# Performance work log

Hardware: AMD Instinct MI355X
Metric: run time of the kernel (lower is better)

Reference implementation:

```python
import jax, jax.numpy as jnp
import numpy as np

N_NODES = 100000
N_EDGES = 600000
D = 128
N_LAYERS = 3
N_GRAPHS = 64
LN_EPS = 1e-5


def setup_inputs() -> dict:
    key = jax.random.key(0)
    ks = jax.random.split(key, 10)
    x = jax.random.normal(ks[0], (N_NODES, D), dtype=jnp.float32)
    edge_index = jax.random.randint(ks[1], (2, N_EDGES), 0, N_NODES, dtype=jnp.int32)
    batch_ids = jnp.sort(jax.random.randint(ks[2], (N_NODES,), 0, N_GRAPHS, dtype=jnp.int32))
    s = 1.0 / np.sqrt(D)
    proj_W = jax.random.normal(ks[3], (D, D), dtype=jnp.float32) * s
    proj_b = jnp.zeros((D,), dtype=jnp.float32)
    mlp_W = jax.random.normal(ks[4], (N_LAYERS, D, D), dtype=jnp.float32) * s
    mlp_b = jnp.zeros((N_LAYERS, D), dtype=jnp.float32)
    ln_g = jnp.ones((N_LAYERS, D), dtype=jnp.float32)
    ln_b = jnp.zeros((N_LAYERS, D), dtype=jnp.float32)
    return {"x": x, "edge_index": edge_index, "batch_ids": batch_ids,
            "proj_W": proj_W, "proj_b": proj_b, "mlp_W": mlp_W, "mlp_b": mlp_b,
            "ln_g": ln_g, "ln_b": ln_b}


def _layernorm(h, g, b):
    mu = jnp.mean(h, axis=-1, keepdims=True)
    var = jnp.mean(jnp.square(h - mu), axis=-1, keepdims=True)
    return (h - mu) * jax.lax.rsqrt(var + LN_EPS) * g + b


def reference(x, edge_index, batch_ids, proj_W, proj_b, mlp_W, mlp_b, ln_g, ln_b):
    # proj_in + ReLU (dropout is identity in eval)
    h = jax.nn.relu(x @ proj_W + proj_b)  # [N, D]
    src, dst = edge_index[0], edge_index[1]
    n = h.shape[0]
    for i in range(N_LAYERS):
        # GINConv, eps=0: mlp(h + sum_{j in N(v)} h_j); messages flow src -> dst
        agg = jax.ops.segment_sum(h[src], dst, num_segments=n)  # [N, D]
        h = jax.nn.relu((h + agg) @ mlp_W[i] + mlp_b[i])  # internal MLP: Linear + ReLU
        h = _layernorm(h, ln_g[i], ln_b[i])
    # global mean pool over graphs
    sums = jax.ops.segment_sum(h, batch_ids, num_segments=N_GRAPHS)  # [G, D]
    counts = jax.ops.segment_sum(jnp.ones((n,), h.dtype), batch_ids, num_segments=N_GRAPHS)
    return sums / jnp.maximum(counts, 1.0)[:, None]
```

## Files before the change

kernel.cpp:

```cpp
#include <hip/hip_runtime.h>
#include <hip/hip_bf16.h>

#define NN 100000
#define NE 600000
#define DD 128
#define NL 3
#define NG 64
#define LN_EPS 1e-5f

typedef __attribute__((ext_vector_type(8))) short short8v;
typedef __attribute__((ext_vector_type(8))) unsigned short ushort8v;
typedef __attribute__((ext_vector_type(4))) float f32x4;
typedef unsigned short ushort;
typedef unsigned int uint;

__device__ inline float2 unpk2(uint u) {
  float2 r;
  r.x = __uint_as_float(u << 16);
  r.y = __uint_as_float(u & 0xffff0000u);
  return r;
}

__device__ inline void split2(float ax, float ay, uint& hi2, uint& lo2) {
  const uint ux = __float_as_uint(ax), uy = __float_as_uint(ay);
  hi2 = (ux >> 16) | (uy & 0xffff0000u);
  const float rx = ax - __uint_as_float(ux & 0xffff0000u);
  const float ry = ay - __uint_as_float(uy & 0xffff0000u);
  __hip_bfloat16 bx = __float2bfloat16(rx), by = __float2bfloat16(ry);
  lo2 = (uint)*(ushort*)&bx | ((uint)*(ushort*)&by << 16);
}

__global__ __launch_bounds__(256)
void count_kernel(const int* __restrict__ dst, int* __restrict__ deg) {
  const int e = blockIdx.x * 256 + threadIdx.x;
  if (e < NE) atomicAdd(&deg[dst[e]], 1);
}

__global__ __launch_bounds__(256)
void scan_a(const int* __restrict__ deg, int* __restrict__ off, int* __restrict__ btot) {
  __shared__ int wsum[4];
  const int t = threadIdx.x, lane = t & 63, wid = t >> 6;
  const int base = blockIdx.x * 1024 + t * 4;
  int4 d = {0, 0, 0, 0};
  if (base < NN) d = *(const int4*)(deg + base);
  const int s0 = d.x, s1 = s0 + d.y, s2 = s1 + d.z, s3 = s2 + d.w;
  int v = s3;
#pragma unroll
  for (int o = 1; o < 64; o <<= 1) { const int u = __shfl_up(v, o); if (lane >= o) v += u; }
  if (lane == 63) wsum[wid] = v;
  __syncthreads();
  if (t == 0) {
    int a = 0;
#pragma unroll
    for (int i = 0; i < 4; ++i) { const int x = wsum[i]; wsum[i] = a; a += x; }
    btot[blockIdx.x] = a;
  }
  __syncthreads();
  const int texcl = wsum[wid] + v - s3;
  if (base < NN) {
    const int4 o4 = {texcl, texcl + s0, texcl + s1, texcl + s2};
    *(int4*)(off + base) = o4;
  }
}

__global__ __launch_bounds__(128)
void scan_b(int* __restrict__ btot, int nb) {
  __shared__ int wsum[2];
  const int t = threadIdx.x, lane = t & 63, wid = t >> 6;
  const int x = (t < nb) ? btot[t] : 0;
  int v = x;
#pragma unroll
  for (int o = 1; o < 64; o <<= 1) { const int u = __shfl_up(v, o); if (lane >= o) v += u; }
  if (lane == 63) wsum[wid] = v;
  __syncthreads();
  if (t == 0) { const int w0 = wsum[0]; wsum[0] = 0; wsum[1] = w0; }
  __syncthreads();
  const int excl = wsum[wid] + v - x;
  if (t < nb) btot[t] = excl;
}

__global__ __launch_bounds__(256)
void scan_c(int* __restrict__ off, const int* __restrict__ btot) {
  const int i = blockIdx.x * 256 + threadIdx.x;
  if (i < NN) off[i] += btot[i >> 10];
}

__global__ __launch_bounds__(256)
void fill_kernel(const int* __restrict__ src, const int* __restrict__ dst,
                 int* __restrict__ off, int* __restrict__ csr) {
  const int e = blockIdx.x * 256 + threadIdx.x;
  if (e < NE) {
    const int p = atomicAdd(&off[dst[e]], 1);
    csr[p] = src[e];
  }
}

__global__ __launch_bounds__(256)
void wprep_kernel(const float* __restrict__ projW, const float* __restrict__ mlpW,
                  ushort* __restrict__ Wp) {
  const int tid = blockIdx.x * 256 + threadIdx.x;
  const int lane = tid & 63;
  const int fid = tid >> 6;
  const int mat = fid >> 5;
  const int rem = fid & 31;
  const int kk = rem >> 3, nf = rem & 7;
  const float* W = (mat == 0) ? projW : (mlpW + (size_t)(mat - 1) * DD * DD);
  const int k0 = kk * 32 + (lane >> 4) * 8;
  const int col = nf * 16 + (lane & 15);
  ushort8v hv, lv;
#pragma unroll
  for (int j = 0; j < 8; ++j) {
    const float f = W[(size_t)(k0 + j) * DD + col];
    __hip_bfloat16 bh = __float2bfloat16(f);
    __hip_bfloat16 bl = __float2bfloat16(f - __bfloat162float(bh));
    hv[j] = *(ushort*)&bh;
    lv[j] = *(ushort*)&bl;
  }
  ushort* base = Wp + (size_t)mat * 32768;
  *(ushort8v*)(base + ((size_t)((kk * 8 + nf) * 2 + 0) * 64 + lane) * 8) = hv;
  *(ushort8v*)(base + ((size_t)((kk * 8 + nf) * 2 + 1) * 64 + lane) * 8) = lv;
}

template<int MODE>
__global__ __launch_bounds__(256, 4)
void gemm_node(const float* __restrict__ Xf, const ushort* __restrict__ Hin,
               const int* __restrict__ csr, const int* __restrict__ offE,
               const ushort* __restrict__ Wp, const float* __restrict__ bias,
               const float* __restrict__ lng, const float* __restrict__ lnb,
               ushort* __restrict__ Hout) {
  __align__(16) __shared__ ushort AH[64 * 128];
  __align__(16) __shared__ ushort AL[64 * 128];
  const int t = threadIdx.x, lane = t & 63, w = t >> 6;
  const int q = lane >> 4;
  const int ll = lane & 15;
  const int r0 = blockIdx.x * 64;
  const int qbase = r0 + w * 16 + q * 4;
  const uint4* __restrict__ hu4 = (const uint4*)Hin;

  if constexpr (MODE == 1) {
    int offv = 0;
    if (ll < 5) {
      const int gi = qbase - 1 + ll;
      const int gic = gi < 0 ? 0 : (gi > NN - 1 ? NN - 1 : gi);
      offv = (gi < 0) ? 0 : offE[gic];
    }
    int idxA, idxB;
    {
      const int j = ll & 7;
      const int rA = ll >> 3;
      const int a0 = __shfl(offv, q * 16 + rA);
      const int a1 = __shfl(offv, q * 16 + rA + 1);
      int ii = a0 + j;
      int iic = ii < NE ? ii : NE - 1;
      const int cv = csr[iic];
      idxA = (ii < a1) ? cv : NN;
      const int rB = 2 + (ll >> 3);
      const int b0 = __shfl(offv, q * 16 + rB);
      const int b1 = __shfl(offv, q * 16 + rB + 1);
      ii = b0 + j;
      iic = ii < NE ? ii : NE - 1;
      const int cw = csr[iic];
      idxB = (ii < b1) ? cw : NN;
    }

    uint4 gA[9], gB[9];
    auto ISSUE = [&](int s, uint4 (&g)[9]) {
      const int bl = q * 16 + ((s & 1) << 3);
      const int srcv = (s < 2) ? idxA : idxB;
#pragma unroll
      for (int j = 0; j < 8; ++j) {
        const int id = __shfl(srcv, bl + j);
        g[j] = hu4[id * 16 + ll];
      }
      const int v = qbase + s;
      const int sid = (v < NN) ? v : NN;
      g[8] = hu4[sid * 16 + ll];
    };
    auto CONSUME = [&](int s, uint4 (&g)[9]) {
      float4 ev = {0.f, 0.f, 0.f, 0.f}, od = {0.f, 0.f, 0.f, 0.f};
#pragma unroll
      for (int j = 0; j < 9; ++j) {
        const float2 a = unpk2(g[j].x), b = unpk2(g[j].y);
        const float2 c = unpk2(g[j].z), d = unpk2(g[j].w);
        ev.x += a.x; od.x += a.y; ev.y += b.x; od.y += b.y;
        ev.z += c.x; od.z += c.y; ev.w += d.x; od.w += d.y;
      }
      const int i0s = __shfl(offv, q * 16 + s);
      const int i1s = __shfl(offv, q * 16 + s + 1);
      int i = i0s + 8;
#pragma unroll 1
      while (i < i1s) {
#pragma unroll
        for (int jj = 0; jj < 4; ++jj) {
          const int ii = i + jj;
          const int iic = ii < NE ? ii : NE - 1;
          int id = csr[iic];
          id = (ii < i1s) ? id : NN;
          const uint4 gg = hu4[id * 16 + ll];
          const float2 a = unpk2(gg.x), b = unpk2(gg.y);
          const float2 c = unpk2(gg.z), d = unpk2(gg.w);
          ev.x += a.x; od.x += a.y; ev.y += b.x; od.y += b.y;
          ev.z += c.x; od.z += c.y; ev.w += d.x; od.w += d.y;
        }
        i += 4;
      }
      uint h0, l0, h1, l1, h2, l2, h3, l3;
      split2(ev.x, od.x, h0, l0);
      split2(ev.y, od.y, h1, l1);
      split2(ev.z, od.z, h2, l2);
      split2(ev.w, od.w, h3, l3);
      const int row = w * 16 + q * 4 + s;
      const int uoff = (row * 16 + (ll ^ (row & 7))) * 8;
      *(uint4*)&AH[uoff] = make_uint4(h0, h1, h2, h3);
      *(uint4*)&AL[uoff] = make_uint4(l0, l1, l2, l3);
    };

    ISSUE(0, gA);
    ISSUE(1, gB);
    CONSUME(0, gA);
    ISSUE(2, gA);
    CONSUME(1, gB);
    ISSUE(3, gB);
    CONSUME(2, gA);
    CONSUME(3, gB);
  } else {
    const float4* __restrict__ Xf4 = (const float4*)Xf;
    float4 a0, b0, a1, b1;
    auto LOADX = [&](int s, float4& fa, float4& fb) {
      int v = qbase + s;
      v = v < NN ? v : NN - 1;
      fa = Xf4[v * 32 + 2 * ll];
      fb = Xf4[v * 32 + 2 * ll + 1];
    };
    auto STOREX = [&](int s, const float4& fa, const float4& fb) {
      uint h0, l0, h1, l1, h2, l2, h3, l3;
      split2(fa.x, fa.y, h0, l0);
      split2(fa.z, fa.w, h1, l1);
      split2(fb.x, fb.y, h2, l2);
      split2(fb.z, fb.w, h3, l3);
      const int row = w * 16 + q * 4 + s;
      const int uoff = (row * 16 + (ll ^ (row & 7))) * 8;
      *(uint4*)&AH[uoff] = make_uint4(h0, h1, h2, h3);
      *(uint4*)&AL[uoff] = make_uint4(l0, l1, l2, l3);
    };
    LOADX(0, a0, b0);
    LOADX(1, a1, b1);
    STOREX(0, a0, b0);
    LOADX(2, a0, b0);
    STOREX(1, a1, b1);
    LOADX(3, a1, b1);
    STOREX(2, a0, b0);
    STOREX(3, a1, b1);
  }

  f32x4 accv[8];
#pragma unroll
  for (int nf = 0; nf < 8; ++nf) accv[nf] = (f32x4){0.f, 0.f, 0.f, 0.f};
  const int arow = w * 16 + (lane & 15);
  const int qq = lane >> 4;
  const int rx = arow & 7;
#pragma unroll
  for (int kk = 0; kk < 4; ++kk) {
    const int aidx = (arow * 16 + ((kk * 4 + qq) ^ rx)) * 8;
    const short8v ah = *(const short8v*)&AH[aidx];
    const short8v al = *(const short8v*)&AL[aidx];
#pragma unroll
    for (int nf = 0; nf < 8; ++nf) {
      const ushort* bp = Wp + ((size_t)((kk * 8 + nf) * 2) * 64 + lane) * 8;
      const short8v bh = *(const short8v*)bp;
      const short8v bl = *(const short8v*)(bp + 64 * 8);
      accv[nf] = __builtin_amdgcn_mfma_f32_16x16x32_bf16(ah, bh, accv[nf], 0, 0, 0);
      accv[nf] = __builtin_amdgcn_mfma_f32_16x16x32_bf16(al, bh, accv[nf], 0, 0, 0);
      accv[nf] = __builtin_amdgcn_mfma_f32_16x16x32_bf16(ah, bl, accv[nf], 0, 0, 0);
    }
  }

  const int colb = lane & 15;
  float bias8[8], g8[8], q8[8];
#pragma unroll
  for (int nf = 0; nf < 8; ++nf) {
    bias8[nf] = bias[nf * 16 + colb];
    if (MODE == 1) { g8[nf] = lng[nf * 16 + colb]; q8[nf] = lnb[nf * 16 + colb]; }
  }
#pragma unroll
  for (int r = 0; r < 4; ++r) {
    const int grow = r0 + w * 16 + (lane >> 4) * 4 + r;
    float z[8];
    float s = 0.f, s2 = 0.f;
#pragma unroll
    for (int nf = 0; nf < 8; ++nf) {
      z[nf] = fmaxf(accv[nf][r] + bias8[nf], 0.f);
      s += z[nf];
      s2 += z[nf] * z[nf];
    }
    if (MODE == 1) {
#pragma unroll
      for (int o = 1; o < 16; o <<= 1) { s += __shfl_xor(s, o); s2 += __shfl_xor(s2, o); }
      const float mu = s * (1.f / DD);
      const float inv = rsqrtf(s2 * (1.f / DD) - mu * mu + LN_EPS);
#pragma unroll
      for (int nf = 0; nf < 8; ++nf) z[nf] = (z[nf] - mu) * inv * g8[nf] + q8[nf];
    }
    if (grow < NN) {
      ushort* yp = Hout + grow * DD + colb;
#pragma unroll
      for (int nf = 0; nf < 8; ++nf) {
        __hip_bfloat16 b = __float2bfloat16(z[nf]);
        yp[nf * 16] = *(ushort*)&b;
      }
    }
  }
}

__global__ __launch_bounds__(64)
void pool_kernel(const ushort* __restrict__ h, const int* __restrict__ batch,
                 float* __restrict__ sums, float* __restrict__ counts) {
  const int c = threadIdx.x;
  const int base = blockIdx.x * 64;
  const int end = (base + 64 < NN) ? base + 64 : NN;
  const uint* __restrict__ hu = (const uint*)h;
  int cur = batch[base];
  float a0 = 0.f, a1 = 0.f, cnt = 0.f;
  for (int r = base; r < end; ++r) {
    const int g = batch[r];
    if (g != cur) {
      __hip_atomic_fetch_add(&sums[cur * DD + 2 * c], a0, __ATOMIC_RELAXED, __HIP_MEMORY_SCOPE_AGENT);
      __hip_atomic_fetch_add(&sums[cur * DD + 2 * c + 1], a1, __ATOMIC_RELAXED, __HIP_MEMORY_SCOPE_AGENT);
      if (c == 0)
        __hip_atomic_fetch_add(&counts[cur], cnt, __ATOMIC_RELAXED, __HIP_MEMORY_SCOPE_AGENT);
      a0 = 0.f; a1 = 0.f; cnt = 0.f; cur = g;
    }
    const float2 f = unpk2(hu[r * 64 + c]);
    a0 += f.x; a1 += f.y; cnt += 1.f;
  }
  __hip_atomic_fetch_add(&sums[cur * DD + 2 * c], a0, __ATOMIC_RELAXED, __HIP_MEMORY_SCOPE_AGENT);
  __hip_atomic_fetch_add(&sums[cur * DD + 2 * c + 1], a1, __ATOMIC_RELAXED, __HIP_MEMORY_SCOPE_AGENT);
  if (c == 0)
    __hip_atomic_fetch_add(&counts[cur], cnt, __ATOMIC_RELAXED, __HIP_MEMORY_SCOPE_AGENT);
}

__global__ __launch_bounds__(256)
void finalize_kernel(const float* __restrict__ sums, const float* __restrict__ counts,
                     float* __restrict__ out) {
  const int i = blockIdx.x * 256 + threadIdx.x;
  if (i >= NG * DD) return;
  out[i] = sums[i] / fmaxf(counts[i >> 7], 1.f);
}

extern "C" void kernel_launch(void* const* d_in, const int* in_sizes, int n_in,
                              void* d_out, int out_size, void* d_ws, size_t ws_size,
                              hipStream_t stream) {
  const float* x     = (const float*)d_in[0];
  const int*   ei    = (const int*)d_in[1];
  const int*   batch = (const int*)d_in[2];
  const float* projW = (const float*)d_in[3];
  const float* projb = (const float*)d_in[4];
  const float* mlpW  = (const float*)d_in[5];
  const float* mlpb  = (const float*)d_in[6];
  const float* lng   = (const float*)d_in[7];
  const float* lnb   = (const float*)d_in[8];
  float* out = (float*)d_out;

  char* ws = (char*)d_ws;
  ushort* hA    = (ushort*)(ws + 0);
  ushort* hB    = (ushort*)(ws + 25600256);
  int*   csr    = (int*)   (ws + 51200512);
  int*   deg    = (int*)   (ws + 53600512);
  int*   off    = (int*)   (ws + 54000512);
  int*   btot   = (int*)   (ws + 54400512);
  ushort* Wp    = (ushort*)(ws + 54401024);
  float* sums   = (float*) (ws + 54663168);
  float* counts = (float*) (ws + 54695936);

  const int* src = ei;
  const int* dst = ei + NE;

  hipMemsetAsync(hA + (size_t)NN * DD, 0, DD * sizeof(ushort), stream);
  hipMemsetAsync(hB + (size_t)NN * DD, 0, DD * sizeof(ushort), stream);

  hipMemsetAsync(deg, 0, NN * sizeof(int), stream);
  count_kernel<<<(NE + 255) / 256, 256, 0, stream>>>(dst, deg);
  scan_a<<<(NN + 1023) / 1024, 256, 0, stream>>>(deg, off, btot);
  scan_b<<<1, 128, 0, stream>>>(btot, (NN + 1023) / 1024);
  scan_c<<<(NN + 255) / 256, 256, 0, stream>>>(off, btot);
  fill_kernel<<<(NE + 255) / 256, 256, 0, stream>>>(src, dst, off, csr);

  wprep_kernel<<<32, 256, 0, stream>>>(projW, mlpW, Wp);

  const int gemm_blocks = (NN + 63) / 64;

  gemm_node<0><<<gemm_blocks, 256, 0, stream>>>(
      x, nullptr, nullptr, nullptr, Wp, projb, nullptr, nullptr, hA);

  ushort* hin = hA;
  ushort* hout = hB;
  for (int l = 0; l < NL; ++l) {
    gemm_node<1><<<gemm_blocks, 256, 0, stream>>>(
        nullptr, hin, csr, off, Wp + (size_t)(1 + l) * 32768,
        mlpb + (size_t)l * DD, lng + (size_t)l * DD, lnb + (size_t)l * DD, hout);
    ushort* tmp = hin; hin = hout; hout = tmp;
  }

  hipMemsetAsync(sums, 0, (size_t)(NG * DD + NG) * sizeof(float), stream);
  pool_kernel<<<(NN + 63) / 64, 64, 0, stream>>>(hin, batch, sums, counts);
  finalize_kernel<<<(NG * DD + 255) / 256, 256, 0, stream>>>(sums, counts, out);
}
```

Before: 268.7 us.

## Split GEMM tile by output columns per wave with B double-buffering and cross-wave LayerNorm

The fused MLP GEMM kernel now has each wave own 32 output columns across all 64 rows of the block, instead of 16 rows across all 128 columns. Each wave therefore loads only a quarter of the weight fragments from global memory, and it prefetches the next k-step's weight fragments while the current one computes. Because a row is now spread over four waves, the LayerNorm statistics are reduced through shared memory with extra barriers. The cost is more LDS reads of the A tile, since every wave reads all rows, and added synchronization in the epilogue.

After: 277.7 us. 3.3% more time.

```diff
diff --git a/kernel.cpp b/kernel.cpp
--- a/kernel.cpp
+++ b/kernel.cpp
@@ -252,63 +252,115 @@
     STOREX(2, a0, b0);
     STOREX(3, a1, b1);
   }
-
-  f32x4 accv[8];
-#pragma unroll
-  for (int nf = 0; nf < 8; ++nf) accv[nf] = (f32x4){0.f, 0.f, 0.f, 0.f};
-  const int arow = w * 16 + (lane & 15);
-  const int qq = lane >> 4;
-  const int rx = arow & 7;
+  __syncthreads();
+
+  f32x4 acc[4][2];
+#pragma unroll
+  for (int rg = 0; rg < 4; ++rg)
+#pragma unroll
+    for (int n = 0; n < 2; ++n) acc[rg][n] = (f32x4){0.f, 0.f, 0.f, 0.f};
+
+  auto LDB = [&](int kk, int nf2, short8v& bh, short8v& bl) {
+    const ushort* bp = Wp + (((kk * 8 + 2 * w + nf2) * 2) * 64 + lane) * 8;
+    bh = *(const short8v*)bp;
+    bl = *(const short8v*)(bp + 512);
+  };
+
+  short8v bh0[2], bl0[2], bh1[2], bl1[2];
+  LDB(0, 0, bh0[0], bl0[0]);
+  LDB(0, 1, bh0[1], bl0[1]);
 #pragma unroll
   for (int kk = 0; kk < 4; ++kk) {
-    const int aidx = (arow * 16 + ((kk * 4 + qq) ^ rx)) * 8;
-    const short8v ah = *(const short8v*)&AH[aidx];
-    const short8v al = *(const short8v*)&AL[aidx];
-#pragma unroll
-    for (int nf = 0; nf < 8; ++nf) {
-      const ushort* bp = Wp + ((size_t)((kk * 8 + nf) * 2) * 64 + lane) * 8;
-      const short8v bh = *(const short8v*)bp;
-      const short8v bl = *(const short8v*)(bp + 64 * 8);
-      accv[nf] = __builtin_amdgcn_mfma_f32_16x16x32_bf16(ah, bh, accv[nf], 0, 0, 0);
-      accv[nf] = __builtin_amdgcn_mfma_f32_16x16x32_bf16(al, bh, accv[nf], 0, 0, 0);
-      accv[nf] = __builtin_amdgcn_mfma_f32_16x16x32_bf16(ah, bl, accv[nf], 0, 0, 0);
+    short8v (&bhc)[2] = (kk & 1) ? bh1 : bh0;
+    short8v (&blc)[2] = (kk & 1) ? bl1 : bl0;
+    short8v (&bhn)[2] = (kk & 1) ? bh0 : bh1;
+    short8v (&bln)[2] = (kk & 1) ? bl0 : bl1;
+    if (kk < 3) {
+      LDB(kk + 1, 0, bhn[0], bln[0]);
+      LDB(kk + 1, 1, bhn[1], bln[1]);
     }
-  }
-
-  const int colb = lane & 15;
-  float bias8[8], g8[8], q8[8];
-#pragma unroll
-  for (int nf = 0; nf < 8; ++nf) {
-    bias8[nf] = bias[nf * 16 + colb];
-    if (MODE == 1) { g8[nf] = lng[nf * 16 + colb]; q8[nf] = lnb[nf * 16 + colb]; }
-  }
-#pragma unroll
-  for (int r = 0; r < 4; ++r) {
-    const int grow = r0 + w * 16 + (lane >> 4) * 4 + r;
-    float z[8];
-    float s = 0.f, s2 = 0.f;
-#pragma unroll
-    for (int nf = 0; nf < 8; ++nf) {
-      z[nf] = fmaxf(accv[nf][r] + bias8[nf], 0.f);
-      s += z[nf];
-      s2 += z[nf] * z[nf];
+#pragma unroll
+    for (int rg = 0; rg < 4; ++rg) {
+      const int arow = rg * 16 + ll;
+      const int aidx = (arow * 16 + ((kk * 4 + q) ^ (arow & 7))) * 8;
+      const short8v ah = *(const short8v*)&AH[aidx];
+      const short8v al = *(const short8v*)&AL[aidx];
+#pragma unroll
+      for (int n = 0; n < 2; ++n) {
+        acc[rg][n] = __builtin_amdgcn_mfma_f32_16x16x32_bf16(ah, bhc[n], acc[rg][n], 0, 0, 0);
+        acc[rg][n] = __builtin_amdgcn_mfma_f32_16x16x32_bf16(al, bhc[n], acc[rg][n], 0, 0, 0);
+        acc[rg][n] = __builtin_amdgcn_mfma_f32_16x16x32_bf16(ah, blc[n], acc[rg][n], 0, 0, 0);
+      }
     }
-    if (MODE == 1) {
-#pragma unroll
-      for (int o = 1; o < 16; o <<= 1) { s += __shfl_xor(s, o); s2 += __shfl_xor(s2, o); }
-      const float mu = s * (1.f / DD);
-      const float inv = rsqrtf(s2 * (1.f / DD) - mu * mu + LN_EPS);
-#pragma unroll
-      for (int nf = 0; nf < 8; ++nf) z[nf] = (z[nf] - mu) * inv * g8[nf] + q8[nf];
-    }
-    if (grow < NN) {
-      ushort* yp = Hout + grow * DD + colb;
-#pragma unroll
-      for (int nf = 0; nf < 8; ++nf) {
-        __hip_bfloat16 b = __float2bfloat16(z[nf]);
-        yp[nf * 16] = *(ushort*)&b;
-      }
-    }
+  }
+
+  float b2[2], g2[2], q2[2];
+#pragma unroll
+  for (int n = 0; n < 2; ++n) {
+    const int col = (2 * w + n) * 16 + ll;
+    b2[n] = bias[col];
+    if (MODE == 1) { g2[n] = lng[col]; q2[n] = lnb[col]; }
+  }
+
+#pragma unroll
+  for (int rg = 0; rg < 4; ++rg)
+#pragma unroll
+    for (int r = 0; r < 4; ++r)
+#pragma unroll
+      for (int n = 0; n < 2; ++n)
+        acc[rg][n][r] = fmaxf(acc[rg][n][r] + b2[n], 0.f);
+
+  if constexpr (MODE == 1) {
+    float2 (*lnbuf)[4] = (float2(*)[4])AH;
+    __syncthreads();
+#pragma unroll
+    for (int rg = 0; rg < 4; ++rg)
+#pragma unroll
+      for (int r = 0; r < 4; ++r) {
+        float s = acc[rg][0][r] + acc[rg][1][r];
+        float s2 = acc[rg][0][r] * acc[rg][0][r] + acc[rg][1][r] * acc[rg][1][r];
+#pragma unroll
+        for (int o = 1; o < 16; o <<= 1) { s += __shfl_xor(s, o); s2 += __shfl_xor(s2, o); }
+        if (ll == 0) lnbuf[rg * 16 + q * 4 + r][w] = make_float2(s, s2);
+      }
+    __syncthreads();
+#pragma unroll
+    for (int rg = 0; rg < 4; ++rg)
+#pragma unroll
+      for (int r = 0; r < 4; ++r) {
+        const int row = rg * 16 + q * 4 + r;
+        const float4 pa = *(const float4*)&lnbuf[row][0];
+        const float4 pb = *(const float4*)&lnbuf[row][2];
+        const float s = pa.x + pa.z + pb.x + pb.z;
+        const float s2 = pa.y + pa.w + pb.y + pb.w;
+        const float mu = s * (1.f / DD);
+        const float inv = rsqrtf(s2 * (1.f / DD) - mu * mu + LN_EPS);
+        const int grow = r0 + row;
+        if (grow < NN) {
+          ushort* yp = Hout + grow * DD + 2 * w * 16 + ll;
+#pragma unroll
+          for (int n = 0; n < 2; ++n) {
+            const float z = (acc[rg][n][r] - mu) * inv * g2[n] + q2[n];
+            __hip_bfloat16 b = __float2bfloat16(z);
+            yp[n * 16] = *(ushort*)&b;
+          }
+        }
+      }
+  } else {
+#pragma unroll
+    for (int rg = 0; rg < 4; ++rg)
+#pragma unroll
+      for (int r = 0; r < 4; ++r) {
+        const int grow = r0 + rg * 16 + q * 4 + r;
+        if (grow < NN) {
+          ushort* yp = Hout + grow * DD + 2 * w * 16 + ll;
+#pragma unroll
+          for (int n = 0; n < 2; ++n) {
+            __hip_bfloat16 b = __float2bfloat16(acc[rg][n][r]);
+            yp[n * 16] = *(ushort*)&b;
+          }
+        }
+      }
   }
 }
 
```

## Precompute padded ELL neighbor table and restructure gather and MFMA pipelining

Applied to the files above, without the earlier changes.

Adds an ell_kernel that packs, per node, the first 8 neighbor ids plus the CSR start and degree into a 10-int record. The aggregation kernels can then load all gather indices with one vectorised read instead of chained offset-to-CSR lookups. The gather is reorganised so each 16-lane group handles rows spaced 16 apart, with double-buffered batches of 6 loads and a separate tail loop for nodes of degree above 8. The X-load path is remapped, and the MFMA loop now prefetches the next B fragment while the current one is used. The cost is an extra preprocessing kernel, more workspace, and a new explicit __syncthreads.

After: 304.4 us. 13.3% more time.

```diff
diff --git a/kernel.cpp b/kernel.cpp
--- a/kernel.cpp
+++ b/kernel.cpp
@@ -93,6 +93,21 @@
     const int p = atomicAdd(&off[dst[e]], 1);
     csr[p] = src[e];
   }
+}
+
+__global__ __launch_bounds__(256)
+void ell_kernel(const int* __restrict__ off, const int* __restrict__ csr,
+                int* __restrict__ ell) {
+  const int v = blockIdx.x * 256 + threadIdx.x;
+  if (v >= NN) return;
+  const int i0 = v ? off[v - 1] : 0;
+  const int i1 = off[v];
+  const int dg = i1 - i0;
+  int* ep = ell + v * 10;
+#pragma unroll
+  for (int s = 0; s < 8; ++s) ep[s] = (s < dg) ? csr[i0 + s] : NN;
+  ep[8] = i0;
+  ep[9] = dg;
 }
 
 __global__ __launch_bounds__(256)
@@ -124,155 +139,159 @@
 template<int MODE>
 __global__ __launch_bounds__(256, 4)
 void gemm_node(const float* __restrict__ Xf, const ushort* __restrict__ Hin,
-               const int* __restrict__ csr, const int* __restrict__ offE,
+               const int* __restrict__ ell, const int* __restrict__ csr,
                const ushort* __restrict__ Wp, const float* __restrict__ bias,
                const float* __restrict__ lng, const float* __restrict__ lnb,
                ushort* __restrict__ Hout) {
   __align__(16) __shared__ ushort AH[64 * 128];
   __align__(16) __shared__ ushort AL[64 * 128];
   const int t = threadIdx.x, lane = t & 63, w = t >> 6;
-  const int q = lane >> 4;
-  const int ll = lane & 15;
   const int r0 = blockIdx.x * 64;
-  const int qbase = r0 + w * 16 + q * 4;
-  const uint4* __restrict__ hu4 = (const uint4*)Hin;
 
   if constexpr (MODE == 1) {
-    int offv = 0;
-    if (ll < 5) {
-      const int gi = qbase - 1 + ll;
-      const int gic = gi < 0 ? 0 : (gi > NN - 1 ? NN - 1 : gi);
-      offv = (gi < 0) ? 0 : offE[gic];
-    }
-    int idxA, idxB;
+    const int qw = t >> 4, ll = t & 15;
+    const uint4* __restrict__ hu4 = (const uint4*)Hin;
+    int2 e = {NN, NN};
+    int2 e2 = {0, 0};
     {
-      const int j = ll & 7;
-      const int rA = ll >> 3;
-      const int a0 = __shfl(offv, q * 16 + rA);
-      const int a1 = __shfl(offv, q * 16 + rA + 1);
-      int ii = a0 + j;
-      int iic = ii < NE ? ii : NE - 1;
-      const int cv = csr[iic];
-      idxA = (ii < a1) ? cv : NN;
-      const int rB = 2 + (ll >> 3);
-      const int b0 = __shfl(offv, q * 16 + rB);
-      const int b1 = __shfl(offv, q * 16 + rB + 1);
-      ii = b0 + j;
-      iic = ii < NE ? ii : NE - 1;
-      const int cw = csr[iic];
-      idxB = (ii < b1) ? cw : NN;
-    }
-
-    uint4 gA[9], gB[9];
-    auto ISSUE = [&](int s, uint4 (&g)[9]) {
-      const int bl = q * 16 + ((s & 1) << 3);
-      const int srcv = (s < 2) ? idxA : idxB;
-#pragma unroll
-      for (int j = 0; j < 8; ++j) {
-        const int id = __shfl(srcv, bl + j);
-        g[j] = hu4[id * 16 + ll];
+      const int gr_l = r0 + qw + 16 * (ll >> 2);
+      if (gr_l < NN) {
+        e = *(const int2*)&ell[gr_l * 10 + (ll & 3) * 2];
+        if ((ll & 3) == 0) e2 = *(const int2*)&ell[gr_l * 10 + 8];
       }
-      const int v = qbase + s;
-      const int sid = (v < NN) ? v : NN;
-      g[8] = hu4[sid * 16 + ll];
+    }
+    float a[4][8];
+#pragma unroll
+    for (int k = 0; k < 4; ++k)
+#pragma unroll
+      for (int j = 0; j < 8; ++j) a[k][j] = 0.f;
+
+    uint4 gA[6], gB[6];
+    auto IDX = [&](int k, int s) -> int {
+      if (s == 8) { const int gr = r0 + qw + 16 * k; return gr < NN ? gr : NN; }
+      const int src = (k << 2) + (s >> 1);
+      const int ex = __shfl(e.x, src, 16);
+      const int ey = __shfl(e.y, src, 16);
+      return (s & 1) ? ey : ex;
     };
-    auto CONSUME = [&](int s, uint4 (&g)[9]) {
-      float4 ev = {0.f, 0.f, 0.f, 0.f}, od = {0.f, 0.f, 0.f, 0.f};
-#pragma unroll
-      for (int j = 0; j < 9; ++j) {
-        const float2 a = unpk2(g[j].x), b = unpk2(g[j].y);
-        const float2 c = unpk2(g[j].z), d = unpk2(g[j].w);
-        ev.x += a.x; od.x += a.y; ev.y += b.x; od.y += b.y;
-        ev.z += c.x; od.z += c.y; ev.w += d.x; od.w += d.y;
+    auto ISSUE = [&](int g, uint4 (&gb)[6]) {
+#pragma unroll
+      for (int m = 0; m < 6; ++m) {
+        const int task = g * 6 + m;
+        const int id = IDX(task & 3, task >> 2);
+        gb[m] = hu4[id * 16 + ll];
       }
-      const int i0s = __shfl(offv, q * 16 + s);
-      const int i1s = __shfl(offv, q * 16 + s + 1);
-      int i = i0s + 8;
+    };
+    auto CONS = [&](int g, uint4 (&gb)[6]) {
+#pragma unroll
+      for (int m = 0; m < 6; ++m) {
+        const int k = (g * 6 + m) & 3;
+        const float2 p0 = unpk2(gb[m].x), p1 = unpk2(gb[m].y);
+        const float2 p2 = unpk2(gb[m].z), p3 = unpk2(gb[m].w);
+        a[k][0] += p0.x; a[k][1] += p0.y;
+        a[k][2] += p1.x; a[k][3] += p1.y;
+        a[k][4] += p2.x; a[k][5] += p2.y;
+        a[k][6] += p3.x; a[k][7] += p3.y;
+      }
+    };
+    ISSUE(0, gA); ISSUE(1, gB);
+    CONS(0, gA);  ISSUE(2, gA);
+    CONS(1, gB);  ISSUE(3, gB);
+    CONS(2, gA);  ISSUE(4, gA);
+    CONS(3, gB);  ISSUE(5, gB);
+    CONS(4, gA);  CONS(5, gB);
+
+#pragma unroll
+    for (int k = 0; k < 4; ++k) {
+      const int i0k = __shfl(e2.x, k << 2, 16);
+      const int dgk = __shfl(e2.y, k << 2, 16);
+      if (dgk > 8) {
+        const int end = i0k + dgk;
 #pragma unroll 1
-      while (i < i1s) {
-#pragma unroll
-        for (int jj = 0; jj < 4; ++jj) {
-          const int ii = i + jj;
-          const int iic = ii < NE ? ii : NE - 1;
-          int id = csr[iic];
-          id = (ii < i1s) ? id : NN;
-          const uint4 gg = hu4[id * 16 + ll];
-          const float2 a = unpk2(gg.x), b = unpk2(gg.y);
-          const float2 c = unpk2(gg.z), d = unpk2(gg.w);
-          ev.x += a.x; od.x += a.y; ev.y += b.x; od.y += b.y;
-          ev.z += c.x; od.z += c.y; ev.w += d.x; od.w += d.y;
+        for (int i = i0k + 8; i < end; i += 2) {
+          const int ia = csr[i];
+          const int ibr = i + 1 < end ? csr[i + 1] : NN;
+          const uint4 ga = hu4[ia * 16 + ll];
+          const uint4 gb_ = hu4[ibr * 16 + ll];
+          const float2 q0 = unpk2(ga.x), q1 = unpk2(ga.y), q2 = unpk2(ga.z), q3 = unpk2(ga.w);
+          const float2 r0_ = unpk2(gb_.x), r1 = unpk2(gb_.y), r2 = unpk2(gb_.z), r3 = unpk2(gb_.w);
+          a[k][0] += q0.x + r0_.x; a[k][1] += q0.y + r0_.y;
+          a[k][2] += q1.x + r1.x;  a[k][3] += q1.y + r1.y;
+          a[k][4] += q2.x + r2.x;  a[k][5] += q2.y + r2.y;
+          a[k][6] += q3.x + r3.x;  a[k][7] += q3.y + r3.y;
         }
-        i += 4;
       }
+    }
+
+#pragma unroll
+    for (int k = 0; k < 4; ++k) {
       uint h0, l0, h1, l1, h2, l2, h3, l3;
-      split2(ev.x, od.x, h0, l0);
-      split2(ev.y, od.y, h1, l1);
-      split2(ev.z, od.z, h2, l2);
-      split2(ev.w, od.w, h3, l3);
-      const int row = w * 16 + q * 4 + s;
+      split2(a[k][0], a[k][1], h0, l0);
+      split2(a[k][2], a[k][3], h1, l1);
+      split2(a[k][4], a[k][5], h2, l2);
+      split2(a[k][6], a[k][7], h3, l3);
+      const int row = qw + 16 * k;
       const int uoff = (row * 16 + (ll ^ (row & 7))) * 8;
       *(uint4*)&AH[uoff] = make_uint4(h0, h1, h2, h3);
       *(uint4*)&AL[uoff] = make_uint4(l0, l1, l2, l3);
-    };
-
-    ISSUE(0, gA);
-    ISSUE(1, gB);
-    CONSUME(0, gA);
-    ISSUE(2, gA);
-    CONSUME(1, gB);
-    ISSUE(3, gB);
-    CONSUME(2, gA);
-    CONSUME(3, gB);
+    }
   } else {
+    const int row = t >> 2;
+    const int c = t & 3;
+    int v = r0 + row;
+    v = v < NN ? v : NN - 1;
     const float4* __restrict__ Xf4 = (const float4*)Xf;
-    float4 a0, b0, a1, b1;
-    auto LOADX = [&](int s, float4& fa, float4& fb) {
-      int v = qbase + s;
-      v = v < NN ? v : NN - 1;
-      fa = Xf4[v * 32 + 2 * ll];
-      fb = Xf4[v * 32 + 2 * ll + 1];
-    };
-    auto STOREX = [&](int s, const float4& fa, const float4& fb) {
+    float4 fa[4], fb[4];
+#pragma unroll
+    for (int m = 0; m < 4; ++m) {
+      fa[m] = Xf4[v * 32 + c * 8 + 2 * m];
+      fb[m] = Xf4[v * 32 + c * 8 + 2 * m + 1];
+    }
+#pragma unroll
+    for (int m = 0; m < 4; ++m) {
       uint h0, l0, h1, l1, h2, l2, h3, l3;
-      split2(fa.x, fa.y, h0, l0);
-      split2(fa.z, fa.w, h1, l1);
-      split2(fb.x, fb.y, h2, l2);
-      split2(fb.z, fb.w, h3, l3);
-      const int row = w * 16 + q * 4 + s;
-      const int uoff = (row * 16 + (ll ^ (row & 7))) * 8;
+      split2(fa[m].x, fa[m].y, h0, l0);
+      split2(fa[m].z, fa[m].w, h1, l1);
+      split2(fb[m].x, fb[m].y, h2, l2);
+      split2(fb[m].z, fb[m].w, h3, l3);
+      const int llv = c * 4 + m;
+      const int uoff = (row * 16 + (llv ^ (row & 7))) * 8;
       *(uint4*)&AH[uoff] = make_uint4(h0, h1, h2, h3);
       *(uint4*)&AL[uoff] = make_uint4(l0, l1, l2, l3);
-    };
-    LOADX(0, a0, b0);
-    LOADX(1, a1, b1);
-    STOREX(0, a0, b0);
-    LOADX(2, a0, b0);
-    STOREX(1, a1, b1);
-    LOADX(3, a1, b1);
-    STOREX(2, a0, b0);
-    STOREX(3, a1, b1);
-  }
+    }
+  }
+  __syncthreads();
 
   f32x4 accv[8];
 #pragma unroll
   for (int nf = 0; nf < 8; ++nf) accv[nf] = (f32x4){0.f, 0.f, 0.f, 0.f};
   const int arow = w * 16 + (lane & 15);
-  const int qq = lane >> 4;
+  const int q = lane >> 4;
   const int rx = arow & 7;
-#pragma unroll
-  for (int kk = 0; kk < 4; ++kk) {
-    const int aidx = (arow * 16 + ((kk * 4 + qq) ^ rx)) * 8;
-    const short8v ah = *(const short8v*)&AH[aidx];
-    const short8v al = *(const short8v*)&AL[aidx];
-#pragma unroll
-    for (int nf = 0; nf < 8; ++nf) {
-      const ushort* bp = Wp + ((size_t)((kk * 8 + nf) * 2) * 64 + lane) * 8;
-      const short8v bh = *(const short8v*)bp;
-      const short8v bl = *(const short8v*)(bp + 64 * 8);
-      accv[nf] = __builtin_amdgcn_mfma_f32_16x16x32_bf16(ah, bh, accv[nf], 0, 0, 0);
-      accv[nf] = __builtin_amdgcn_mfma_f32_16x16x32_bf16(al, bh, accv[nf], 0, 0, 0);
-      accv[nf] = __builtin_amdgcn_mfma_f32_16x16x32_bf16(ah, bl, accv[nf], 0, 0, 0);
-    }
+
+  short8v bh[2], bl[2];
+  {
+    const ushort* bp = Wp + ((size_t)0 * 64 + lane) * 8;
+    bh[0] = *(const short8v*)bp;
+    bl[0] = *(const short8v*)(bp + 512);
+  }
+  short8v ah{}, al{};
+#pragma unroll
+  for (int st = 0; st < 32; ++st) {
+    if (st < 31) {
+      const ushort* bp = Wp + ((size_t)((st + 1) * 2) * 64 + lane) * 8;
+      bh[(st + 1) & 1] = *(const short8v*)bp;
+      bl[(st + 1) & 1] = *(const short8v*)(bp + 512);
+    }
+    const int kk = st >> 3, nf = st & 7;
+    if (nf == 0) {
+      const int aidx = (arow * 16 + ((kk * 4 + q) ^ rx)) * 8;
+      ah = *(const short8v*)&AH[aidx];
+      al = *(const short8v*)&AL[aidx];
+    }
+    accv[nf] = __builtin_amdgcn_mfma_f32_16x16x32_bf16(ah, bh[st & 1], accv[nf], 0, 0, 0);
+    accv[nf] = __builtin_amdgcn_mfma_f32_16x16x32_bf16(al, bh[st & 1], accv[nf], 0, 0, 0);
+    accv[nf] = __builtin_amdgcn_mfma_f32_16x16x32_bf16(ah, bl[st & 1], accv[nf], 0, 0, 0);
   }
 
   const int colb = lane & 15;
@@ -365,12 +384,13 @@
   ushort* hA    = (ushort*)(ws + 0);
   ushort* hB    = (ushort*)(ws + 25600256);
   int*   csr    = (int*)   (ws + 51200512);
-  int*   deg    = (int*)   (ws + 53600512);
-  int*   off    = (int*)   (ws + 54000512);
-  int*   btot   = (int*)   (ws + 54400512);
-  ushort* Wp    = (ushort*)(ws + 54401024);
-  float* sums   = (float*) (ws + 54663168);
-  float* counts = (float*) (ws + 54695936);
+  int*   ell    = (int*)   (ws + 53600512);
+  int*   deg    = (int*)   (ws + 57600512);
+  int*   off    = (int*)   (ws + 58000512);
+  int*   btot   = (int*)   (ws + 58400512);
+  ushort* Wp    = (ushort*)(ws + 58401024);
+  float* sums   = (float*) (ws + 58663168);
+  float* counts = (float*) (ws + 58695936);
 
   const int* src = ei;
   const int* dst = ei + NE;
@@ -384,6 +404,7 @@
   scan_b<<<1, 128, 0, stream>>>(btot, (NN + 1023) / 1024);
   scan_c<<<(NN + 255) / 256, 256, 0, stream>>>(off, btot);
   fill_kernel<<<(NE + 255) / 256, 256, 0, stream>>>(src, dst, off, csr);
+  ell_kernel<<<(NN + 255) / 256, 256, 0, stream>>>(off, csr, ell);
 
   wprep_kernel<<<32, 256, 0, stream>>>(projW, mlpW, Wp);
 
@@ -396,7 +417,7 @@
   ushort* hout = hB;
   for (int l = 0; l < NL; ++l) {
     gemm_node<1><<<gemm_blocks, 256, 0, stream>>>(
-        nullptr, hin, csr, off, Wp + (size_t)(1 + l) * 32768,
+        nullptr, hin, ell, csr, Wp + (size_t)(1 + l) * 32768,
         mlpb + (size_t)l * DD, lng + (size_t)l * DD, lnb + (size_t)l * DD, hout);
     ushort* tmp = hin; hin = hout; hout = tmp;
   }
```
